# Kernel optimization log

Measured on AMD Instinct MI355X. Metric: run time of the kernel, lower is better.

Reference implementation:

```python
import jax, jax.numpy as jnp
import numpy as np

L, D, H, V, S, HID = 4, 1024, 16, 32000, 2048, 2816
HD = D // H  # 64
EPS = 1e-5


def setup_inputs() -> dict:
    key = jax.random.key(0)
    ks = jax.random.split(key, 10)
    s = 0.02  # init scale for numerical sanity; math is unaffected
    return {
        "tokens": jax.random.randint(ks[0], (1, S), 0, V),
        "emb": jax.random.normal(ks[1], (V, D), jnp.float32) * s,
        "wq": jax.random.normal(ks[2], (L, D, D), jnp.float32) * s,
        "wk": jax.random.normal(ks[3], (L, D, D), jnp.float32) * s,
        "wv": jax.random.normal(ks[4], (L, D, D), jnp.float32) * s,
        "wo": jax.random.normal(ks[5], (L, D, D), jnp.float32) * s,
        "w1": jax.random.normal(ks[6], (L, HID, D), jnp.float32) * s,
        "w2": jax.random.normal(ks[7], (L, D, HID), jnp.float32) * s,
        "w3": jax.random.normal(ks[8], (L, HID, D), jnp.float32) * s,
        "attn_norm_w": jnp.ones((L, D), jnp.float32),
        "ffn_norm_w": jnp.ones((L, D), jnp.float32),
        "final_norm_w": jnp.ones((D,), jnp.float32),
    }


def _rmsnorm(x, w):
    return x * jax.lax.rsqrt(jnp.mean(x * x, axis=-1, keepdims=True) + EPS) * w


def _rope(x, cos, sin):
    # x: [B,S,H,HD]; interleaved pairs (..., -1, 2) as in apply_rotary_emb
    xr, xi = x[..., 0::2], x[..., 1::2]
    outr = xr * cos - xi * sin
    outi = xr * sin + xi * cos
    return jnp.stack([outr, outi], axis=-1).reshape(x.shape)


def reference(tokens, emb, wq, wk, wv, wo, w1, w2, w3, attn_norm_w, ffn_norm_w, final_norm_w):
    # precompute_freqs_cis(head_dim, seq)
    inv_freq = 1.0 / (10000.0 ** (jnp.arange(0, HD, 2, dtype=jnp.float32) / HD))
    fr = jnp.outer(jnp.arange(S, dtype=jnp.float32), inv_freq)  # [S, HD/2]
    cos = jnp.cos(fr)[None, :, None, :]
    sin = jnp.sin(fr)[None, :, None, :]
    mask = jnp.triu(jnp.full((S, S), -jnp.inf, jnp.float32), k=1)
    scale = 1.0 / jnp.sqrt(jnp.float32(HD))

    h = emb[tokens]  # [B,S,D] embedding lookup (dropout p=0 -> identity)
    B = h.shape[0]

    def block(h, p):
        Wq, Wk, Wv, Wo, W1, W2, W3, anw, fnw = p
        x = _rmsnorm(h, anw)
        q = (x @ Wq.T).reshape(B, S, H, HD)
        k = (x @ Wk.T).reshape(B, S, H, HD)
        v = (x @ Wv.T).reshape(B, S, H, HD)
        q = _rope(q, cos, sin)
        k = _rope(k, cos, sin)
        q, k, v = (t.transpose(0, 2, 1, 3) for t in (q, k, v))  # [B,H,S,HD]
        scores = jnp.einsum("bhqd,bhkd->bhqk", q, k) * scale + mask
        attn = jax.nn.softmax(scores, axis=-1)
        o = jnp.einsum("bhqk,bhkd->bhqd", attn, v)
        o = o.transpose(0, 2, 1, 3).reshape(B, S, D)
        h = h + o @ Wo.T
        y = _rmsnorm(h, fnw)
        ff = (jax.nn.silu(y @ W1.T) * (y @ W3.T)) @ W2.T
        return h + ff, None

    h, _ = jax.lax.scan(block, h, (wq, wk, wv, wo, w1, w2, w3, attn_norm_w, ffn_norm_w))
    h = _rmsnorm(h, final_norm_w)
    logits = h[:, -1:, :] @ emb.T  # output weight tied to tok_embeddings; last position only
    return logits
```

## Files before the change

### kernel.cpp

```cpp
#include <hip/hip_runtime.h>

#define LNUM 4
#define DIM 1024
#define NH 16
#define VOCAB 32000
#define SEQ 2048
#define HIDD 2816

typedef _Float16 f16;
typedef _Float16 h8_t __attribute__((ext_vector_type(8)));
typedef _Float16 h4_t __attribute__((ext_vector_type(4)));
typedef float f4_t __attribute__((ext_vector_type(4)));

#define MFMA(a, b, c) __builtin_amdgcn_mfma_f32_16x16x32_f16(a, b, c, 0, 0, 0)

__device__ __forceinline__ void async16(void* lds, const void* g) {
  __builtin_amdgcn_global_load_lds(
      (const __attribute__((address_space(1))) void*)g,
      (__attribute__((address_space(3))) void*)lds, 16, 0, 0);
}

template <int N>
__device__ __forceinline__ float ror16(float x) {
  int r = __builtin_amdgcn_update_dpp(0, __builtin_bit_cast(int, x),
                                      0x120 | N, 0xF, 0xF, true);
  return __builtin_bit_cast(float, r);
}
__device__ __forceinline__ float rmax16(float v) {
  v = fmaxf(v, ror16<1>(v));
  v = fmaxf(v, ror16<2>(v));
  v = fmaxf(v, ror16<4>(v));
  v = fmaxf(v, ror16<8>(v));
  return v;
}
__device__ __forceinline__ float rsum16(float v) {
  v += ror16<1>(v);
  v += ror16<2>(v);
  v += ror16<4>(v);
  v += ror16<8>(v);
  return v;
}
__device__ __forceinline__ float qswap(float x) {
  int r = __builtin_amdgcn_update_dpp(0, __builtin_bit_cast(int, x), 0xB1,
                                      0xF, 0xF, true);
  return __builtin_bit_cast(float, r);
}

__global__ __launch_bounds__(256) void cast_layer_k(
    const float* __restrict__ wq, const float* __restrict__ wk,
    const float* __restrict__ wv, const float* __restrict__ wo,
    const float* __restrict__ w1, const float* __restrict__ w3,
    const float* __restrict__ w2, f16* __restrict__ wqkv,
    f16* __restrict__ wod, f16* __restrict__ w13, f16* __restrict__ w2d) {
  const int DD4c = DIM * DIM / 4, HD4c = HIDD * DIM / 4;
  int i = blockIdx.x * 256 + threadIdx.x;
  const float* s;
  f16* d;
  int si, di;
  if (i < 3 * DD4c) {
    d = wqkv;
    di = i;
    if (i < DD4c) {
      s = wq; si = i;
    } else if (i < 2 * DD4c) {
      s = wk; si = i - DD4c;
    } else {
      s = wv; si = i - 2 * DD4c;
    }
  } else if (i < 4 * DD4c) {
    s = wo; si = i - 3 * DD4c; d = wod; di = si;
  } else if (i < 4 * DD4c + HD4c) {
    s = w1; si = i - 4 * DD4c; d = w13; di = si;
  } else if (i < 4 * DD4c + 2 * HD4c) {
    s = w3; si = i - 4 * DD4c - HD4c; d = w13; di = si + HD4c;
  } else {
    s = w2; si = i - 4 * DD4c - 2 * HD4c; d = w2d; di = si;
  }
  float4 v = ((const float4*)s)[si];
  ((h4_t*)d)[di] = (h4_t){(f16)v.x, (f16)v.y, (f16)v.z, (f16)v.w};
}

__global__ __launch_bounds__(256) void embed_k(const int* __restrict__ tok,
                                               const float* __restrict__ emb,
                                               float* __restrict__ h) {
  const int s = blockIdx.x, t = threadIdx.x;
  ((float4*)(h + (size_t)s * DIM))[t] =
      ((const float4*)(emb + (size_t)tok[s] * DIM))[t];
}

__global__ void rope_tab_k(float* __restrict__ tab) {
  int i = blockIdx.x * 256 + threadIdx.x;
  if (i >= SEQ * 32) return;
  int s = i >> 5, f = i & 31;
  float inv = powf(10000.f, -(float)f * (1.f / 32.f));
  float a = (float)s * inv;
  float sn, c;
  sincosf(a, &sn, &c);
  tab[i * 2] = c;
  tab[i * 2 + 1] = sn;
}

__global__ __launch_bounds__(256) void rmsnorm_k(const float* __restrict__ h,
                                                 const float* __restrict__ w,
                                                 f16* __restrict__ out) {
  const int s = blockIdx.x, t = threadIdx.x;
  float4 v = ((const float4*)(h + (size_t)s * DIM))[t];
  float ss = v.x * v.x + v.y * v.y + v.z * v.z + v.w * v.w;
#pragma unroll
  for (int d = 1; d < 64; d <<= 1) ss += __shfl_xor(ss, d);
  __shared__ float red[4];
  if ((t & 63) == 0) red[t >> 6] = ss;
  __syncthreads();
  float tot = red[0] + red[1] + red[2] + red[3];
  float sc = rsqrtf(tot * (1.f / (float)DIM) + 1e-5f);
  float4 wv = ((const float4*)w)[t];
  ((h4_t*)(out + (size_t)s * DIM))[t] =
      (h4_t){(f16)(v.x * sc * wv.x), (f16)(v.y * sc * wv.y),
             (f16)(v.z * sc * wv.z), (f16)(v.w * sc * wv.w)};
}

__global__ __launch_bounds__(256) void final_norm_k(const float* __restrict__ h,
                                                    const float* __restrict__ w,
                                                    float* __restrict__ hn) {
  const int t = threadIdx.x;
  float4 v = ((const float4*)(h + (size_t)(SEQ - 1) * DIM))[t];
  float ss = v.x * v.x + v.y * v.y + v.z * v.z + v.w * v.w;
#pragma unroll
  for (int d = 1; d < 64; d <<= 1) ss += __shfl_xor(ss, d);
  __shared__ float red[4];
  if ((t & 63) == 0) red[t >> 6] = ss;
  __syncthreads();
  float tot = red[0] + red[1] + red[2] + red[3];
  float sc = rsqrtf(tot * (1.f / (float)DIM) + 1e-5f);
  float4 wv = ((const float4*)w)[t];
  ((float4*)hn)[t] = make_float4(v.x * sc * wv.x, v.y * sc * wv.y,
                                 v.z * sc * wv.z, v.w * sc * wv.w);
}

__global__ __launch_bounds__(256) void logits_k(const float* __restrict__ hn,
                                                const float* __restrict__ emb,
                                                float* __restrict__ out) {
  const int v = blockIdx.x * 4 + (threadIdx.x >> 6);
  const int lane = threadIdx.x & 63;
  const float4* er = (const float4*)(emb + (size_t)v * DIM);
  const float4* hr = (const float4*)hn;
  float s = 0.f;
#pragma unroll
  for (int i = 0; i < 4; i++) {
    float4 a = er[lane + i * 64];
    float4 b = hr[lane + i * 64];
    s += a.x * b.x + a.y * b.y + a.z * b.z + a.w * b.w;
  }
#pragma unroll
  for (int d = 1; d < 64; d <<= 1) s += __shfl_xor(s, d);
  if (lane == 0) out[v] = s;
}

__global__ __launch_bounds__(256) void silu_k(const f16* __restrict__ g13,
                                              f16* __restrict__ t) {
  int c = blockIdx.x * 256 + threadIdx.x;
  int s = blockIdx.y;
  float g = (float)g13[(size_t)s * (2 * HIDD) + c];
  float u = (float)g13[(size_t)s * (2 * HIDD) + HIDD + c];
  float r = g / (1.f + __expf(-g)) * u;
  t[(size_t)s * HIDD + c] = (f16)r;
}

__global__ __launch_bounds__(256) void transpose_v(const f16* __restrict__ qkv,
                                                   f16* __restrict__ vT) {
  __shared__ f16 tile[32][34];
  int bs = blockIdx.x * 32;
  int bc = blockIdx.y * 32;
  int tx = threadIdx.x & 31, ty = threadIdx.x >> 5;
#pragma unroll
  for (int i = ty; i < 32; i += 8)
    tile[i][tx] = qkv[(size_t)(bs + i) * 3072 + 2048 + bc + tx];
  __syncthreads();
#pragma unroll
  for (int i = ty; i < 32; i += 8)
    vT[(size_t)(bc + i) * SEQ + bs + tx] = tile[tx][i];
}


#define GEMM_PIPE_LOOP(KLEN, LDSTRIDE)                                       \
  {                                                                          \
    async16(lA, gA);                                                         \
    async16(lA + 64 * 32, gA + (size_t)64 * (LDSTRIDE));                     \
    async16(lB, gB);                                                         \
    async16(lB + 64 * 32, gB + (size_t)64 * (LDSTRIDE));                     \
    for (int k0 = 0; k0 < (KLEN); k0 += 32) {                                \
      const int cur = (k0 >> 5) & 1;                                         \
      if (k0 + 32 < (KLEN)) {                                                \
        const int nxt = cur ^ 1;                                             \
        async16(lA + nxt * 4096, gA + k0 + 32);                              \
        async16(lA + nxt * 4096 + 64 * 32,                                   \
                gA + (size_t)64 * (LDSTRIDE) + k0 + 32);                     \
        async16(lB + nxt * 4096, gB + k0 + 32);                              \
        async16(lB + nxt * 4096 + 64 * 32,                                   \
                gB + (size_t)64 * (LDSTRIDE) + k0 + 32);                     \
        asm volatile("s_waitcnt vmcnt(4)" ::: "memory");                     \
      } else {                                                               \
        asm volatile("s_waitcnt vmcnt(0)" ::: "memory");                     \
      }                                                                      \
      asm volatile("s_barrier" ::: "memory");                                \
      const f16* As_c = As + cur * 4096;                                     \
      const f16* Bs_c = Bs + cur * 4096;                                     \
      h8_t af[4], bfr[4];                                                    \
      _Pragma("unroll") for (int m = 0; m < 4; m++) af[m] =                  \
          *(const h8_t*)(As_c + (wr * 64 + m * 16 + lr) * 32 +               \
                         ((lk ^ sw) << 3));                                  \
      _Pragma("unroll") for (int n = 0; n < 4; n++) bfr[n] =                 \
          *(const h8_t*)(Bs_c + (wc * 64 + n * 16 + lr) * 32 +               \
                         ((lk ^ sw) << 3));                                  \
      _Pragma("unroll") for (int m = 0; m < 4; m++)                          \
          _Pragma("unroll") for (int n = 0; n < 4; n++) acc[m][n] =          \
              MFMA(af[m], bfr[n], acc[m][n]);                                \
      asm volatile("s_waitcnt lgkmcnt(0)" ::: "memory");                     \
      asm volatile("s_barrier" ::: "memory");                                \
    }                                                                        \
  }

template <int EPI>
__global__ __launch_bounds__(256) void gemm_bt(const f16* __restrict__ A,
                                               const f16* __restrict__ B,
                                               void* __restrict__ Cout, int M,
                                               int N, int K) {
  __shared__ __align__(16) f16 As[2 * 128 * 32];
  __shared__ __align__(16) f16 Bs[2 * 128 * 32];
  const int t = threadIdx.x;
  const int lane = t & 63;
  const int wave = t >> 6;
  const int wr = wave >> 1, wc = wave & 1;
  const int bm = blockIdx.x, bn = blockIdx.y;
  const int lr = lane & 15, lk = lane >> 4;
  const int sw = (lr >> 1) & 3;

  const int srow = t >> 2;
  const int scol = (((t & 3) ^ ((t >> 3) & 3))) * 8;
  const f16* gA = A + (size_t)(bm * 128 + srow) * K + scol;
  const f16* gB = B + (size_t)(bn * 128 + srow) * K + scol;
  f16* lA = As + t * 8;
  f16* lB = Bs + t * 8;

  f4_t acc[4][4];
#pragma unroll
  for (int m = 0; m < 4; m++)
#pragma unroll
    for (int n = 0; n < 4; n++) acc[m][n] = {0.f, 0.f, 0.f, 0.f};

  GEMM_PIPE_LOOP(K, K)

  const int orow = bm * 128 + wr * 64 + lk * 4;
  const int ocol = bn * 128 + wc * 64 + lr;
#pragma unroll
  for (int m = 0; m < 4; m++)
#pragma unroll
    for (int n = 0; n < 4; n++)
#pragma unroll
      for (int j = 0; j < 4; j++) {
        int r = orow + m * 16 + j;
        int c = ocol + n * 16;
        if (EPI == 0) {
          ((f16*)Cout)[(size_t)r * N + c] = (f16)acc[m][n][j];
        } else {
          float* pC = (float*)Cout + (size_t)r * N + c;
          *pC += acc[m][n][j];
        }
      }
}

__global__ __launch_bounds__(256) void gemm_qkv(const f16* __restrict__ A,
                                                const f16* __restrict__ B,
                                                f16* __restrict__ C,
                                                const float* __restrict__ tab) {
  const int N = 3 * DIM, K = DIM;
  __shared__ __align__(16) f16 As[2 * 128 * 32];
  __shared__ __align__(16) f16 Bs[2 * 128 * 32];
  const int t = threadIdx.x;
  const int lane = t & 63;
  const int wave = t >> 6;
  const int wr = wave >> 1, wc = wave & 1;
  const int bm = blockIdx.x, bn = blockIdx.y;
  const int lr = lane & 15, lk = lane >> 4;
  const int sw = (lr >> 1) & 3;

  const int srow = t >> 2;
  const int scol = (((t & 3) ^ ((t >> 3) & 3))) * 8;
  const f16* gA = A + (size_t)(bm * 128 + srow) * K + scol;
  const f16* gB = B + (size_t)(bn * 128 + srow) * K + scol;
  f16* lA = As + t * 8;
  f16* lB = Bs + t * 8;

  f4_t acc[4][4];
#pragma unroll
  for (int m = 0; m < 4; m++)
#pragma unroll
    for (int n = 0; n < 4; n++) acc[m][n] = {0.f, 0.f, 0.f, 0.f};

  GEMM_PIPE_LOOP(K, K)

  const int orow = bm * 128 + wr * 64 + lk * 4;
  const int ocol = bn * 128 + wc * 64 + lr;
  const float ssign = (lr & 1) ? 1.f : -1.f;
#pragma unroll
  for (int m = 0; m < 4; m++)
#pragma unroll
    for (int n = 0; n < 4; n++) {
      const int c = ocol + n * 16;
      const bool qk = c < 2048;
      const int f = (n * 16 + lr) >> 1;
#pragma unroll
      for (int j = 0; j < 4; j++) {
        int r = orow + m * 16 + j;
        float sv = acc[m][n][j];
        float pa = qswap(sv);
        if (qk) {
          float2 cs = ((const float2*)tab)[r * 32 + f];
          sv = sv * cs.x + pa * cs.y * ssign;
        }
        C[(size_t)r * N + c] = (f16)sv;
      }
    }
}

__global__ __launch_bounds__(256) void gemm_skp(const f16* __restrict__ A,
                                                const f16* __restrict__ B,
                                                float* __restrict__ Cp, int N,
                                                int ld, int Ks) {
  __shared__ __align__(16) f16 As[2 * 128 * 32];
  __shared__ __align__(16) f16 Bs[2 * 128 * 32];
  const int t = threadIdx.x;
  const int lane = t & 63;
  const int wave = t >> 6;
  const int wr = wave >> 1, wc = wave & 1;
  const int bm = blockIdx.x, bn = blockIdx.y, bk = blockIdx.z;
  const int lr = lane & 15, lk = lane >> 4;
  const int sw = (lr >> 1) & 3;

  const f16* Ao = A + (size_t)bk * Ks;
  const f16* Bo = B + (size_t)bk * Ks;
  float* Cout = Cp + (size_t)bk * gridDim.x * 128 * N;

  const int srow = t >> 2;
  const int scol = (((t & 3) ^ ((t >> 3) & 3))) * 8;
  const f16* gA = Ao + (size_t)(bm * 128 + srow) * ld + scol;
  const f16* gB = Bo + (size_t)(bn * 128 + srow) * ld + scol;
  f16* lA = As + t * 8;
  f16* lB = Bs + t * 8;

  f4_t acc[4][4];
#pragma unroll
  for (int m = 0; m < 4; m++)
#pragma unroll
    for (int n = 0; n < 4; n++) acc[m][n] = {0.f, 0.f, 0.f, 0.f};

  GEMM_PIPE_LOOP(Ks, ld)

  const int orow = bm * 128 + wr * 64 + lk * 4;
  const int ocol = bn * 128 + wc * 64 + lr;
#pragma unroll
  for (int m = 0; m < 4; m++)
#pragma unroll
    for (int n = 0; n < 4; n++)
#pragma unroll
      for (int j = 0; j < 4; j++)
        Cout[(size_t)(orow + m * 16 + j) * N + ocol + n * 16] = acc[m][n][j];
}

__global__ __launch_bounds__(256) void sk_reduce_k(const float* __restrict__ p,
                                                   float* __restrict__ h,
                                                   int n4) {
  int i = blockIdx.x * 256 + threadIdx.x;
  if (i >= n4) return;
  float4 a = ((const float4*)p)[i];
  float4 b = ((const float4*)p)[i + n4];
  float4 c = ((float4*)h)[i];
  c.x += a.x + b.x;
  c.y += a.y + b.y;
  c.z += a.z + b.z;
  c.w += a.w + b.w;
  ((float4*)h)[i] = c;
}

__global__ __launch_bounds__(256) void attn_k(const f16* __restrict__ qkv,
                                              const f16* __restrict__ vT,
                                              f16* __restrict__ o) {
  const int hh = blockIdx.x;
  const int qb = blockIdx.y;
  const int tid = threadIdx.x;
  const int wave = tid >> 6;
  const int lane = tid & 63;
  const int lr = lane & 15, lk = lane >> 4;
  const int q0 = qb * 32;
  __shared__ __align__(16) char P[4][4096];
  __shared__ float MBml[3][64][16];
  __shared__ f16 MBo[3][64][32];

  h8_t qf[2][2];
#pragma unroll
  for (int m = 0; m < 2; m++)
#pragma unroll
    for (int ks = 0; ks < 2; ks++)
      qf[m][ks] = *(const h8_t*)(qkv + (size_t)(q0 + m * 16 + lr) * 3072 +
                                 hh * 64 + ks * 32 + lk * 8);

  float mrow[2][4], lsum[2][4];
  f4_t oacc[2][4];
#pragma unroll
  for (int m = 0; m < 2; m++)
#pragma unroll
    for (int j = 0; j < 4; j++) {
      mrow[m][j] = -1e30f;
      lsum[m][j] = 0.f;
    }
#pragma unroll
  for (int m = 0; m < 2; m++)
#pragma unroll
    for (int n = 0; n < 4; n++) oacc[m][n] = {0.f, 0.f, 0.f, 0.f};

  const int ntiles = (qb >> 1) + 1;
  char* Pw = P[wave];
  for (int kt = wave; kt < ntiles; kt += 4) {
    f4_t sacc[2][4];
#pragma unroll
    for (int m = 0; m < 2; m++)
#pragma unroll
      for (int n = 0; n < 4; n++) sacc[m][n] = {0.f, 0.f, 0.f, 0.f};
#pragma unroll
    for (int ks = 0; ks < 2; ks++) {
      h8_t kf[4];
#pragma unroll
      for (int n = 0; n < 4; n++)
        kf[n] = *(const h8_t*)(qkv + (size_t)(kt * 64 + n * 16 + lr) * 3072 +
                               1024 + hh * 64 + ks * 32 + lk * 8);
#pragma unroll
      for (int m = 0; m < 2; m++)
#pragma unroll
        for (int n = 0; n < 4; n++)
          sacc[m][n] = MFMA(qf[m][ks], kf[n], sacc[m][n]);
    }
    const bool lastt = (kt == ntiles - 1);
    float pv[2][4][4];
#pragma unroll
    for (int m = 0; m < 2; m++)
#pragma unroll
      for (int n = 0; n < 4; n++)
#pragma unroll
        for (int j = 0; j < 4; j++) {
          float sv = sacc[m][n][j] * 0.125f;
          if (lastt && (kt * 64 + n * 16 + lr) > (q0 + m * 16 + lk * 4 + j))
            sv = -1e30f;
          pv[m][n][j] = sv;
        }
#pragma unroll
    for (int m = 0; m < 2; m++)
#pragma unroll
      for (int j = 0; j < 4; j++) {
        float mx = fmaxf(fmaxf(pv[m][0][j], pv[m][1][j]),
                         fmaxf(pv[m][2][j], pv[m][3][j]));
        mx = rmax16(mx);
        float mnew = fmaxf(mrow[m][j], mx);
        float corr = __expf(mrow[m][j] - mnew);
        mrow[m][j] = mnew;
        float rs = 0.f;
#pragma unroll
        for (int n = 0; n < 4; n++) {
          float pe = __expf(pv[m][n][j] - mnew);
          pv[m][n][j] = pe;
          rs += pe;
        }
        rs = rsum16(rs);
        lsum[m][j] = lsum[m][j] * corr + rs;
#pragma unroll
        for (int n = 0; n < 4; n++) oacc[m][n][j] *= corr;
      }
#pragma unroll
    for (int m = 0; m < 2; m++)
#pragma unroll
      for (int n = 0; n < 4; n++)
#pragma unroll
        for (int j = 0; j < 4; j++) {
          int r = m * 16 + lk * 4 + j, c = n * 16 + lr;
          int off = (r * 128 + c * 2) ^ ((r & 7) << 4);
          *(f16*)(Pw + off) = (f16)pv[m][n][j];
        }
#pragma unroll
    for (int ks = 0; ks < 2; ks++) {
      h8_t pf[2], vf[4];
#pragma unroll
      for (int m = 0; m < 2; m++) {
        int r = m * 16 + lr;
        int off = (r * 128 + ks * 64 + lk * 16) ^ ((r & 7) << 4);
        pf[m] = *(const h8_t*)(Pw + off);
      }
#pragma unroll
      for (int n = 0; n < 4; n++)
        vf[n] = *(const h8_t*)(vT + (size_t)(hh * 64 + n * 16 + lr) * SEQ +
                               kt * 64 + ks * 32 + lk * 8);
#pragma unroll
      for (int m = 0; m < 2; m++)
#pragma unroll
        for (int n = 0; n < 4; n++)
          oacc[m][n] = MFMA(pf[m], vf[n], oacc[m][n]);
    }
  }

  if (wave > 0) {
    float* dml = &MBml[wave - 1][lane][0];
    f16* doo = &MBo[wave - 1][lane][0];
#pragma unroll
    for (int m = 0; m < 2; m++)
#pragma unroll
      for (int j = 0; j < 4; j++) {
        dml[m * 4 + j] = mrow[m][j];
        dml[8 + m * 4 + j] = lsum[m][j];
      }
#pragma unroll
    for (int m = 0; m < 2; m++)
#pragma unroll
      for (int n = 0; n < 4; n++)
#pragma unroll
        for (int j = 0; j < 4; j++)
          doo[m * 16 + n * 4 + j] = (f16)oacc[m][n][j];
  }
  __syncthreads();
  if (wave == 0) {
#pragma unroll
    for (int m = 0; m < 2; m++)
#pragma unroll
      for (int j = 0; j < 4; j++) {
        float M = mrow[m][j];
#pragma unroll
        for (int w = 0; w < 3; w++) M = fmaxf(M, MBml[w][lane][m * 4 + j]);
        float sc0 = __expf(mrow[m][j] - M);
        float L = lsum[m][j] * sc0;
        float scw[3];
#pragma unroll
        for (int w = 0; w < 3; w++) {
          scw[w] = __expf(MBml[w][lane][m * 4 + j] - M);
          L += MBml[w][lane][8 + m * 4 + j] * scw[w];
        }
        float invL = 1.f / L;
#pragma unroll
        for (int n = 0; n < 4; n++) {
          float val = oacc[m][n][j] * sc0;
#pragma unroll
          for (int w = 0; w < 3; w++)
            val += (float)MBo[w][lane][m * 16 + n * 4 + j] * scw[w];
          o[(size_t)(q0 + m * 16 + lk * 4 + j) * DIM + hh * 64 + n * 16 + lr] =
              (f16)(val * invL);
        }
      }
  }
}

extern "C" void kernel_launch(void* const* d_in, const int* in_sizes, int n_in,
                              void* d_out, int out_size, void* d_ws,
                              size_t ws_size, hipStream_t stream) {
  (void)in_sizes; (void)n_in; (void)out_size; (void)ws_size;
  const int* tokens = (const int*)d_in[0];
  const float* emb = (const float*)d_in[1];
  const float* wq = (const float*)d_in[2];
  const float* wk = (const float*)d_in[3];
  const float* wv = (const float*)d_in[4];
  const float* wo = (const float*)d_in[5];
  const float* w1 = (const float*)d_in[6];
  const float* w2 = (const float*)d_in[7];
  const float* w3 = (const float*)d_in[8];
  const float* anw = (const float*)d_in[9];
  const float* fnw = (const float*)d_in[10];
  const float* finw = (const float*)d_in[11];
  float* out = (float*)d_out;

  char* p = (char*)d_ws;
  auto alloc = [&](size_t bytes) {
    char* r = p;
    p += (bytes + 255) & ~(size_t)255;
    return r;
  };
  f16* wqkv_l = (f16*)alloc((size_t)3 * DIM * DIM * 2);
  f16* wo_l = (f16*)alloc((size_t)DIM * DIM * 2);
  f16* w13_l = (f16*)alloc((size_t)2 * HIDD * DIM * 2);
  f16* w2_l = (f16*)alloc((size_t)DIM * HIDD * 2);
  float* hbuf = (float*)alloc((size_t)SEQ * DIM * 4);
  f16* x_h = (f16*)alloc((size_t)SEQ * DIM * 2);
  f16* qkv_h = (f16*)alloc((size_t)SEQ * 3 * DIM * 2);
  f16* vT_h = (f16*)alloc((size_t)DIM * SEQ * 2);
  f16* o_h = (f16*)alloc((size_t)SEQ * DIM * 2);
  f16* g13_h = (f16*)alloc((size_t)SEQ * 2 * HIDD * 2);
  f16* t_h = (f16*)alloc((size_t)SEQ * HIDD * 2);
  float* skbuf = (float*)alloc((size_t)2 * SEQ * DIM * 4);
  float* tab = (float*)alloc((size_t)SEQ * 32 * 2 * 4);
  float* hn = (float*)alloc(4096);

  embed_k<<<SEQ, 256, 0, stream>>>(tokens, emb, hbuf);
  rope_tab_k<<<(SEQ * 32 + 255) / 256, 256, 0, stream>>>(tab);

  const int CAST_BLOCKS = (4 * (DIM * DIM / 4) + 3 * (HIDD * DIM / 4)) / 256;
  const int N4 = SEQ * DIM / 4;
  for (int l = 0; l < LNUM; l++) {
    const size_t offDD = (size_t)l * DIM * DIM;
    const size_t offHD = (size_t)l * HIDD * DIM;
    cast_layer_k<<<CAST_BLOCKS, 256, 0, stream>>>(
        wq + offDD, wk + offDD, wv + offDD, wo + offDD, w1 + offHD,
        w3 + offHD, w2 + offHD, wqkv_l, wo_l, w13_l, w2_l);

    rmsnorm_k<<<SEQ, 256, 0, stream>>>(hbuf, anw + (size_t)l * DIM, x_h);
    {
      dim3 g(SEQ / 128, (3 * DIM) / 128);
      gemm_qkv<<<g, 256, 0, stream>>>(x_h, wqkv_l, qkv_h, tab);
    }
    {
      dim3 g(SEQ / 32, DIM / 32);
      transpose_v<<<g, 256, 0, stream>>>(qkv_h, vT_h);
    }
    {
      dim3 g(NH, SEQ / 32);
      attn_k<<<g, 256, 0, stream>>>(qkv_h, vT_h, o_h);
    }
    {
      dim3 g(SEQ / 128, DIM / 128, 2);
      gemm_skp<<<g, 256, 0, stream>>>(o_h, wo_l, skbuf, DIM, DIM, DIM / 2);
      sk_reduce_k<<<(N4 + 255) / 256, 256, 0, stream>>>(skbuf, hbuf, N4);
    }
    rmsnorm_k<<<SEQ, 256, 0, stream>>>(hbuf, fnw + (size_t)l * DIM, x_h);
    {
      dim3 g(SEQ / 128, (2 * HIDD) / 128);
      gemm_bt<0><<<g, 256, 0, stream>>>(x_h, w13_l, g13_h, SEQ, 2 * HIDD, DIM);
    }
    {
      dim3 g(HIDD / 256, SEQ);
      silu_k<<<g, 256, 0, stream>>>(g13_h, t_h);
    }
    {
      dim3 g(SEQ / 128, DIM / 128, 2);
      gemm_skp<<<g, 256, 0, stream>>>(t_h, w2_l, skbuf, DIM, HIDD, HIDD / 2);
      sk_reduce_k<<<(N4 + 255) / 256, 256, 0, stream>>>(skbuf, hbuf, N4);
    }
  }
  final_norm_k<<<1, 256, 0, stream>>>(hbuf, finw, hn);
  logits_k<<<VOCAB / 4, 256, 0, stream>>>(hn, emb, out);
}
```

Baseline: 868.2 us.

## Fuse split-K reduction into RMSNorm and pair causal attention query blocks

The separate split-K reduce kernel is removed: each RMSNorm (and the final norm) now adds the two partial GEMM outputs into the residual itself. Each launch saves a full pass over the residual and partial buffers plus a kernel launch. The attention grid is also halved, and each block processes a short query block and its mirrored long one (63-qb and qb) in sequence, so causal work is balanced across blocks. The cost is fewer attention blocks, each running two passes with extra barriers.

```diff
diff --git a/kernel.cpp b/kernel.cpp
--- a/kernel.cpp
+++ b/kernel.cpp
@@ -119,11 +119,45 @@
              (f16)(v.z * sc * wv.z), (f16)(v.w * sc * wv.w)};
 }
 
-__global__ __launch_bounds__(256) void final_norm_k(const float* __restrict__ h,
-                                                    const float* __restrict__ w,
-                                                    float* __restrict__ hn) {
+__global__ __launch_bounds__(256) void rmsnorm_sk(float* __restrict__ h,
+                                                  const float* __restrict__ p,
+                                                  const float* __restrict__ w,
+                                                  f16* __restrict__ out) {
+  const int s = blockIdx.x, t = threadIdx.x;
+  float4 v = ((const float4*)(h + (size_t)s * DIM))[t];
+  float4 a = ((const float4*)(p + (size_t)s * DIM))[t];
+  float4 b = ((const float4*)(p + (size_t)SEQ * DIM + (size_t)s * DIM))[t];
+  v.x += a.x + b.x;
+  v.y += a.y + b.y;
+  v.z += a.z + b.z;
+  v.w += a.w + b.w;
+  ((float4*)(h + (size_t)s * DIM))[t] = v;
+  float ss = v.x * v.x + v.y * v.y + v.z * v.z + v.w * v.w;
+#pragma unroll
+  for (int d = 1; d < 64; d <<= 1) ss += __shfl_xor(ss, d);
+  __shared__ float red[4];
+  if ((t & 63) == 0) red[t >> 6] = ss;
+  __syncthreads();
+  float tot = red[0] + red[1] + red[2] + red[3];
+  float sc = rsqrtf(tot * (1.f / (float)DIM) + 1e-5f);
+  float4 wv = ((const float4*)w)[t];
+  ((h4_t*)(out + (size_t)s * DIM))[t] =
+      (h4_t){(f16)(v.x * sc * wv.x), (f16)(v.y * sc * wv.y),
+             (f16)(v.z * sc * wv.z), (f16)(v.w * sc * wv.w)};
+}
+
+__global__ __launch_bounds__(256) void final_norm_sk(
+    const float* __restrict__ h, const float* __restrict__ p,
+    const float* __restrict__ w, float* __restrict__ hn) {
   const int t = threadIdx.x;
-  float4 v = ((const float4*)(h + (size_t)(SEQ - 1) * DIM))[t];
+  const size_t row = (size_t)(SEQ - 1) * DIM;
+  float4 v = ((const float4*)(h + row))[t];
+  float4 a = ((const float4*)(p + row))[t];
+  float4 b = ((const float4*)(p + (size_t)SEQ * DIM + row))[t];
+  v.x += a.x + b.x;
+  v.y += a.y + b.y;
+  v.z += a.z + b.z;
+  v.w += a.w + b.w;
   float ss = v.x * v.x + v.y * v.y + v.z * v.z + v.w * v.w;
 #pragma unroll
   for (int d = 1; d < 64; d <<= 1) ss += __shfl_xor(ss, d);
@@ -367,190 +401,181 @@
         Cout[(size_t)(orow + m * 16 + j) * N + ocol + n * 16] = acc[m][n][j];
 }
 
-__global__ __launch_bounds__(256) void sk_reduce_k(const float* __restrict__ p,
-                                                   float* __restrict__ h,
-                                                   int n4) {
-  int i = blockIdx.x * 256 + threadIdx.x;
-  if (i >= n4) return;
-  float4 a = ((const float4*)p)[i];
-  float4 b = ((const float4*)p)[i + n4];
-  float4 c = ((float4*)h)[i];
-  c.x += a.x + b.x;
-  c.y += a.y + b.y;
-  c.z += a.z + b.z;
-  c.w += a.w + b.w;
-  ((float4*)h)[i] = c;
-}
-
 __global__ __launch_bounds__(256) void attn_k(const f16* __restrict__ qkv,
                                               const f16* __restrict__ vT,
                                               f16* __restrict__ o) {
   const int hh = blockIdx.x;
-  const int qb = blockIdx.y;
+  const int qb2 = blockIdx.y;
   const int tid = threadIdx.x;
   const int wave = tid >> 6;
   const int lane = tid & 63;
   const int lr = lane & 15, lk = lane >> 4;
-  const int q0 = qb * 32;
   __shared__ __align__(16) char P[4][4096];
   __shared__ float MBml[3][64][16];
   __shared__ f16 MBo[3][64][32];
-
-  h8_t qf[2][2];
-#pragma unroll
-  for (int m = 0; m < 2; m++)
-#pragma unroll
-    for (int ks = 0; ks < 2; ks++)
-      qf[m][ks] = *(const h8_t*)(qkv + (size_t)(q0 + m * 16 + lr) * 3072 +
-                                 hh * 64 + ks * 32 + lk * 8);
-
-  float mrow[2][4], lsum[2][4];
-  f4_t oacc[2][4];
-#pragma unroll
-  for (int m = 0; m < 2; m++)
-#pragma unroll
-    for (int j = 0; j < 4; j++) {
-      mrow[m][j] = -1e30f;
-      lsum[m][j] = 0.f;
-    }
-#pragma unroll
-  for (int m = 0; m < 2; m++)
-#pragma unroll
-    for (int n = 0; n < 4; n++) oacc[m][n] = {0.f, 0.f, 0.f, 0.f};
-
-  const int ntiles = (qb >> 1) + 1;
   char* Pw = P[wave];
-  for (int kt = wave; kt < ntiles; kt += 4) {
-    f4_t sacc[2][4];
+
+#pragma unroll 1
+  for (int pass = 0; pass < 2; ++pass) {
+    const int qb = pass ? qb2 : (63 - qb2);
+    const int q0 = qb * 32;
+
+    h8_t qf[2][2];
 #pragma unroll
     for (int m = 0; m < 2; m++)
 #pragma unroll
-      for (int n = 0; n < 4; n++) sacc[m][n] = {0.f, 0.f, 0.f, 0.f};
-#pragma unroll
-    for (int ks = 0; ks < 2; ks++) {
-      h8_t kf[4];
-#pragma unroll
-      for (int n = 0; n < 4; n++)
-        kf[n] = *(const h8_t*)(qkv + (size_t)(kt * 64 + n * 16 + lr) * 3072 +
-                               1024 + hh * 64 + ks * 32 + lk * 8);
+      for (int ks = 0; ks < 2; ks++)
+        qf[m][ks] = *(const h8_t*)(qkv + (size_t)(q0 + m * 16 + lr) * 3072 +
+                                   hh * 64 + ks * 32 + lk * 8);
+
+    float mrow[2][4], lsum[2][4];
+    f4_t oacc[2][4];
+#pragma unroll
+    for (int m = 0; m < 2; m++)
+#pragma unroll
+      for (int j = 0; j < 4; j++) {
+        mrow[m][j] = -1e30f;
+        lsum[m][j] = 0.f;
+      }
+#pragma unroll
+    for (int m = 0; m < 2; m++)
+#pragma unroll
+      for (int n = 0; n < 4; n++) oacc[m][n] = {0.f, 0.f, 0.f, 0.f};
+
+    const int ntiles = (qb >> 1) + 1;
+    for (int kt = wave; kt < ntiles; kt += 4) {
+      f4_t sacc[2][4];
 #pragma unroll
       for (int m = 0; m < 2; m++)
 #pragma unroll
+        for (int n = 0; n < 4; n++) sacc[m][n] = {0.f, 0.f, 0.f, 0.f};
+#pragma unroll
+      for (int ks = 0; ks < 2; ks++) {
+        h8_t kf[4];
+#pragma unroll
         for (int n = 0; n < 4; n++)
-          sacc[m][n] = MFMA(qf[m][ks], kf[n], sacc[m][n]);
-    }
-    const bool lastt = (kt == ntiles - 1);
-    float pv[2][4][4];
-#pragma unroll
-    for (int m = 0; m < 2; m++)
-#pragma unroll
-      for (int n = 0; n < 4; n++)
+          kf[n] = *(const h8_t*)(qkv + (size_t)(kt * 64 + n * 16 + lr) * 3072 +
+                                 1024 + hh * 64 + ks * 32 + lk * 8);
+#pragma unroll
+        for (int m = 0; m < 2; m++)
+#pragma unroll
+          for (int n = 0; n < 4; n++)
+            sacc[m][n] = MFMA(qf[m][ks], kf[n], sacc[m][n]);
+      }
+      const bool lastt = (kt == ntiles - 1);
+      float pv[2][4][4];
+#pragma unroll
+      for (int m = 0; m < 2; m++)
+#pragma unroll
+        for (int n = 0; n < 4; n++)
+#pragma unroll
+          for (int j = 0; j < 4; j++) {
+            float sv = sacc[m][n][j] * 0.125f;
+            if (lastt && (kt * 64 + n * 16 + lr) > (q0 + m * 16 + lk * 4 + j))
+              sv = -1e30f;
+            pv[m][n][j] = sv;
+          }
+#pragma unroll
+      for (int m = 0; m < 2; m++)
 #pragma unroll
         for (int j = 0; j < 4; j++) {
-          float sv = sacc[m][n][j] * 0.125f;
-          if (lastt && (kt * 64 + n * 16 + lr) > (q0 + m * 16 + lk * 4 + j))
-            sv = -1e30f;
-          pv[m][n][j] = sv;
+          float mx = fmaxf(fmaxf(pv[m][0][j], pv[m][1][j]),
+                           fmaxf(pv[m][2][j], pv[m][3][j]));
+          mx = rmax16(mx);
+          float mnew = fmaxf(mrow[m][j], mx);
+          float corr = __expf(mrow[m][j] - mnew);
+          mrow[m][j] = mnew;
+          float rs = 0.f;
+#pragma unroll
+          for (int n = 0; n < 4; n++) {
+            float pe = __expf(pv[m][n][j] - mnew);
+            pv[m][n][j] = pe;
+            rs += pe;
+          }
+          rs = rsum16(rs);
+          lsum[m][j] = lsum[m][j] * corr + rs;
+#pragma unroll
+          for (int n = 0; n < 4; n++) oacc[m][n][j] *= corr;
         }
 #pragma unroll
-    for (int m = 0; m < 2; m++)
-#pragma unroll
-      for (int j = 0; j < 4; j++) {
-        float mx = fmaxf(fmaxf(pv[m][0][j], pv[m][1][j]),
-                         fmaxf(pv[m][2][j], pv[m][3][j]));
-        mx = rmax16(mx);
-        float mnew = fmaxf(mrow[m][j], mx);
-        float corr = __expf(mrow[m][j] - mnew);
-        mrow[m][j] = mnew;
-        float rs = 0.f;
-#pragma unroll
-        for (int n = 0; n < 4; n++) {
-          float pe = __expf(pv[m][n][j] - mnew);
-          pv[m][n][j] = pe;
-          rs += pe;
+      for (int m = 0; m < 2; m++)
+#pragma unroll
+        for (int n = 0; n < 4; n++)
+#pragma unroll
+          for (int j = 0; j < 4; j++) {
+            int r = m * 16 + lk * 4 + j, c = n * 16 + lr;
+            int off = (r * 128 + c * 2) ^ ((r & 7) << 4);
+            *(f16*)(Pw + off) = (f16)pv[m][n][j];
+          }
+#pragma unroll
+      for (int ks = 0; ks < 2; ks++) {
+        h8_t pf[2], vf[4];
+#pragma unroll
+        for (int m = 0; m < 2; m++) {
+          int r = m * 16 + lr;
+          int off = (r * 128 + ks * 64 + lk * 16) ^ ((r & 7) << 4);
+          pf[m] = *(const h8_t*)(Pw + off);
         }
-        rs = rsum16(rs);
-        lsum[m][j] = lsum[m][j] * corr + rs;
-#pragma unroll
-        for (int n = 0; n < 4; n++) oacc[m][n][j] *= corr;
+#pragma unroll
+        for (int n = 0; n < 4; n++)
+          vf[n] = *(const h8_t*)(vT + (size_t)(hh * 64 + n * 16 + lr) * SEQ +
+                                 kt * 64 + ks * 32 + lk * 8);
+#pragma unroll
+        for (int m = 0; m < 2; m++)
+#pragma unroll
+          for (int n = 0; n < 4; n++)
+            oacc[m][n] = MFMA(pf[m], vf[n], oacc[m][n]);
       }
-#pragma unroll
-    for (int m = 0; m < 2; m++)
-#pragma unroll
-      for (int n = 0; n < 4; n++)
+    }
+
+    if (wave > 0) {
+      float* dml = &MBml[wave - 1][lane][0];
+      f16* doo = &MBo[wave - 1][lane][0];
+#pragma unroll
+      for (int m = 0; m < 2; m++)
 #pragma unroll
         for (int j = 0; j < 4; j++) {
-          int r = m * 16 + lk * 4 + j, c = n * 16 + lr;
-          int off = (r * 128 + c * 2) ^ ((r & 7) << 4);
-          *(f16*)(Pw + off) = (f16)pv[m][n][j];
+          dml[m * 4 + j] = mrow[m][j];
+          dml[8 + m * 4 + j] = lsum[m][j];
         }
 #pragma unroll
-    for (int ks = 0; ks < 2; ks++) {
-      h8_t pf[2], vf[4];
-#pragma unroll
-      for (int m = 0; m < 2; m++) {
-        int r = m * 16 + lr;
-        int off = (r * 128 + ks * 64 + lk * 16) ^ ((r & 7) << 4);
-        pf[m] = *(const h8_t*)(Pw + off);
-      }
-#pragma unroll
-      for (int n = 0; n < 4; n++)
-        vf[n] = *(const h8_t*)(vT + (size_t)(hh * 64 + n * 16 + lr) * SEQ +
-                               kt * 64 + ks * 32 + lk * 8);
-#pragma unroll
       for (int m = 0; m < 2; m++)
 #pragma unroll
         for (int n = 0; n < 4; n++)
-          oacc[m][n] = MFMA(pf[m], vf[n], oacc[m][n]);
-    }
-  }
-
-  if (wave > 0) {
-    float* dml = &MBml[wave - 1][lane][0];
-    f16* doo = &MBo[wave - 1][lane][0];
-#pragma unroll
-    for (int m = 0; m < 2; m++)
-#pragma unroll
-      for (int j = 0; j < 4; j++) {
-        dml[m * 4 + j] = mrow[m][j];
-        dml[8 + m * 4 + j] = lsum[m][j];
-      }
-#pragma unroll
-    for (int m = 0; m < 2; m++)
-#pragma unroll
-      for (int n = 0; n < 4; n++)
-#pragma unroll
-        for (int j = 0; j < 4; j++)
-          doo[m * 16 + n * 4 + j] = (f16)oacc[m][n][j];
-  }
-  __syncthreads();
-  if (wave == 0) {
-#pragma unroll
-    for (int m = 0; m < 2; m++)
-#pragma unroll
-      for (int j = 0; j < 4; j++) {
-        float M = mrow[m][j];
-#pragma unroll
-        for (int w = 0; w < 3; w++) M = fmaxf(M, MBml[w][lane][m * 4 + j]);
-        float sc0 = __expf(mrow[m][j] - M);
-        float L = lsum[m][j] * sc0;
-        float scw[3];
-#pragma unroll
-        for (int w = 0; w < 3; w++) {
-          scw[w] = __expf(MBml[w][lane][m * 4 + j] - M);
-          L += MBml[w][lane][8 + m * 4 + j] * scw[w];
+#pragma unroll
+          for (int j = 0; j < 4; j++)
+            doo[m * 16 + n * 4 + j] = (f16)oacc[m][n][j];
+    }
+    __syncthreads();
+    if (wave == 0) {
+#pragma unroll
+      for (int m = 0; m < 2; m++)
+#pragma unroll
+        for (int j = 0; j < 4; j++) {
+          float M = mrow[m][j];
+#pragma unroll
+          for (int w = 0; w < 3; w++) M = fmaxf(M, MBml[w][lane][m * 4 + j]);
+          float sc0 = __expf(mrow[m][j] - M);
+          float L = lsum[m][j] * sc0;
+          float scw[3];
+#pragma unroll
+          for (int w = 0; w < 3; w++) {
+            scw[w] = __expf(MBml[w][lane][m * 4 + j] - M);
+            L += MBml[w][lane][8 + m * 4 + j] * scw[w];
+          }
+          float invL = 1.f / L;
+#pragma unroll
+          for (int n = 0; n < 4; n++) {
+            float val = oacc[m][n][j] * sc0;
+#pragma unroll
+            for (int w = 0; w < 3; w++)
+              val += (float)MBo[w][lane][m * 16 + n * 4 + j] * scw[w];
+            o[(size_t)(q0 + m * 16 + lk * 4 + j) * DIM + hh * 64 + n * 16 +
+              lr] = (f16)(val * invL);
+          }
         }
-        float invL = 1.f / L;
-#pragma unroll
-        for (int n = 0; n < 4; n++) {
-          float val = oacc[m][n][j] * sc0;
-#pragma unroll
-          for (int w = 0; w < 3; w++)
-            val += (float)MBo[w][lane][m * 16 + n * 4 + j] * scw[w];
-          o[(size_t)(q0 + m * 16 + lk * 4 + j) * DIM + hh * 64 + n * 16 + lr] =
-              (f16)(val * invL);
-        }
-      }
+    }
+    __syncthreads();
   }
 }
 
@@ -597,7 +622,6 @@
   rope_tab_k<<<(SEQ * 32 + 255) / 256, 256, 0, stream>>>(tab);
 
   const int CAST_BLOCKS = (4 * (DIM * DIM / 4) + 3 * (HIDD * DIM / 4)) / 256;
-  const int N4 = SEQ * DIM / 4;
   for (int l = 0; l < LNUM; l++) {
     const size_t offDD = (size_t)l * DIM * DIM;
     const size_t offHD = (size_t)l * HIDD * DIM;
@@ -605,7 +629,12 @@
         wq + offDD, wk + offDD, wv + offDD, wo + offDD, w1 + offHD,
         w3 + offHD, w2 + offHD, wqkv_l, wo_l, w13_l, w2_l);
 
-    rmsnorm_k<<<SEQ, 256, 0, stream>>>(hbuf, anw + (size_t)l * DIM, x_h);
+    if (l == 0) {
+      rmsnorm_k<<<SEQ, 256, 0, stream>>>(hbuf, anw, x_h);
+    } else {
+      rmsnorm_sk<<<SEQ, 256, 0, stream>>>(hbuf, skbuf, anw + (size_t)l * DIM,
+                                          x_h);
+    }
     {
       dim3 g(SEQ / 128, (3 * DIM) / 128);
       gemm_qkv<<<g, 256, 0, stream>>>(x_h, wqkv_l, qkv_h, tab);
@@ -615,15 +644,15 @@
       transpose_v<<<g, 256, 0, stream>>>(qkv_h, vT_h);
     }
     {
-      dim3 g(NH, SEQ / 32);
+      dim3 g(NH, SEQ / 64);
       attn_k<<<g, 256, 0, stream>>>(qkv_h, vT_h, o_h);
     }
     {
       dim3 g(SEQ / 128, DIM / 128, 2);
       gemm_skp<<<g, 256, 0, stream>>>(o_h, wo_l, skbuf, DIM, DIM, DIM / 2);
-      sk_reduce_k<<<(N4 + 255) / 256, 256, 0, stream>>>(skbuf, hbuf, N4);
-    }
-    rmsnorm_k<<<SEQ, 256, 0, stream>>>(hbuf, fnw + (size_t)l * DIM, x_h);
+    }
+    rmsnorm_sk<<<SEQ, 256, 0, stream>>>(hbuf, skbuf, fnw + (size_t)l * DIM,
+                                        x_h);
     {
       dim3 g(SEQ / 128, (2 * HIDD) / 128);
       gemm_bt<0><<<g, 256, 0, stream>>>(x_h, w13_l, g13_h, SEQ, 2 * HIDD, DIM);
@@ -635,9 +664,8 @@
     {
       dim3 g(SEQ / 128, DIM / 128, 2);
       gemm_skp<<<g, 256, 0, stream>>>(t_h, w2_l, skbuf, DIM, HIDD, HIDD / 2);
-      sk_reduce_k<<<(N4 + 255) / 256, 256, 0, stream>>>(skbuf, hbuf, N4);
     }
   }
-  final_norm_k<<<1, 256, 0, stream>>>(hbuf, finw, hn);
+  final_norm_sk<<<1, 256, 0, stream>>>(hbuf, skbuf, finw, hn);
   logits_k<<<VOCAB / 4, 256, 0, stream>>>(hn, emb, out);
 }
```

Result: faster. 808.4 us (-6.9%).
